# Optimization experiments

Hardware: AMD Instinct MI355X
Metric: run time of the kernel (lower is better)

The kernel has to match this reference:

```python
import jax, jax.numpy as jnp
import numpy as np

B, S, DM, H = 2, 2048, 1024, 16
D = DM // H
SCALE = D ** -0.5


def setup_inputs() -> dict:
    key = jax.random.key(0)
    k1, k2, k3 = jax.random.split(key, 3)
    x = jax.random.normal(k1, (B, S, DM), dtype=jnp.float32)
    w_qkv = jax.random.normal(k2, (DM, 3 * DM), dtype=jnp.float32) * (DM ** -0.5)
    b_qkv = jnp.zeros((3 * DM,), dtype=jnp.float32)
    w_out = jax.random.normal(k3, (DM, DM), dtype=jnp.float32) * (DM ** -0.5)
    b_out = jnp.zeros((DM,), dtype=jnp.float32)
    return {"x": x, "w_qkv": w_qkv, "b_qkv": b_qkv, "w_out": w_out, "b_out": b_out}


def reference(x, w_qkv, b_qkv, w_out, b_out):
    b, n, _ = x.shape
    qkv = x @ w_qkv + b_qkv                          # [b, n, 3*dm]
    q, k, v = jnp.split(qkv, 3, axis=-1)
    # b n (h d) -> b h n d
    split = lambda t: t.reshape(b, n, H, D).transpose(0, 2, 1, 3)
    q, k, v = split(q), split(k), split(v)
    dots = jnp.einsum('bhid,bhjd->bhij', q, k) * SCALE
    # causal (fore) mask: -inf above the diagonal
    causal = jnp.tril(jnp.ones((n, n), dtype=bool))
    dots = jnp.where(causal, dots, -jnp.inf)
    attn = jax.nn.softmax(dots, axis=-1)
    out = jnp.einsum('bhij,bhjd->bhid', attn, v)     # [b, h, n, d]
    out = out.transpose(0, 2, 1, 3).reshape(b, n, H * D)
    return out @ w_out + b_out
```

## Files before the change

kernel.cpp:

```cpp
#include <hip/hip_runtime.h>
#include <hip/hip_bf16.h>

#define NB 2
#define NS 2048
#define NDM 1024
#define NH 16
#define ND 64
#define NM (NB * NS)
#define RS 3072
#define C1 0.1803368801111243f
#define THR_RAW 44.36141956f

typedef __attribute__((ext_vector_type(8))) short bf16x8;
typedef __attribute__((ext_vector_type(4))) float f32x4;

__device__ __forceinline__ unsigned short f2bf(float f) {
    unsigned int u = __float_as_uint(f);
    u += 0x7fffu + ((u >> 16) & 1u);
    return (unsigned short)(u >> 16);
}

__device__ __forceinline__ void gload16(const unsigned short* g, unsigned short* l) {
    __builtin_amdgcn_global_load_lds(
        (const __attribute__((address_space(1))) void*)g,
        (__attribute__((address_space(3))) void*)l, 16, 0, 0);
}

__global__ __launch_bounds__(256)
void convert_bf16(const float* __restrict__ in, unsigned short* __restrict__ out, int n8) {
    int i = blockIdx.x * 256 + threadIdx.x;
    const int stride = gridDim.x * 256;
    for (; i < n8; i += stride) {
        const float4 a = ((const float4*)in)[i * 2];
        const float4 b = ((const float4*)in)[i * 2 + 1];
        bf16x8 v;
        v[0] = (short)f2bf(a.x); v[1] = (short)f2bf(a.y);
        v[2] = (short)f2bf(a.z); v[3] = (short)f2bf(a.w);
        v[4] = (short)f2bf(b.x); v[5] = (short)f2bf(b.y);
        v[6] = (short)f2bf(b.z); v[7] = (short)f2bf(b.w);
        *(bf16x8*)(out + (size_t)i * 8) = v;
    }
}

__global__ __launch_bounds__(256)
void transpose_bf16(const float* __restrict__ W, unsigned short* __restrict__ WT,
                    int K, int N) {
    __shared__ float Ts[64][65];
    const int n0 = blockIdx.x * 64, k0 = blockIdx.y * 64;
    const int t = threadIdx.x;
    {
        const int c4 = (t & 15) * 4;
        #pragma unroll
        for (int p = 0; p < 4; p++) {
            const int r = (t >> 4) + p * 16;
            const float4 v = *(const float4*)(W + (size_t)(k0 + r) * N + n0 + c4);
            Ts[r][c4] = v.x; Ts[r][c4 + 1] = v.y; Ts[r][c4 + 2] = v.z; Ts[r][c4 + 3] = v.w;
        }
    }
    __syncthreads();
    {
        const int cc8 = (t & 7) * 8;
        #pragma unroll
        for (int p = 0; p < 2; p++) {
            const int rr = (t >> 3) + p * 32;
            bf16x8 v;
            #pragma unroll
            for (int j = 0; j < 8; j++) v[j] = (short)f2bf(Ts[cc8 + j][rr]);
            *(bf16x8*)(WT + (size_t)(n0 + rr) * K + k0 + cc8) = v;
        }
    }
}

__global__ __launch_bounds__(256)
void vtrans(const unsigned short* __restrict__ qkvb, unsigned short* __restrict__ vT) {
    __shared__ unsigned short Ts[64][65];
    const int st = blockIdx.x, bh = blockIdx.y;
    const int h = bh & (NH - 1), b = bh >> 4;
    const int t = threadIdx.x;
    {
        const int c8 = (t & 7) * 8;
        #pragma unroll
        for (int p = 0; p < 2; p++) {
            const int r = (t >> 3) + p * 32;
            const unsigned short* src =
                qkvb + (size_t)(b * NS + st * 64 + r) * RS + 2 * NDM + h * ND + c8;
            const bf16x8 v = *(const bf16x8*)src;
            #pragma unroll
            for (int j = 0; j < 8; j++) Ts[r][c8 + j] = (unsigned short)v[j];
        }
    }
    __syncthreads();
    {
        #pragma unroll
        for (int i = 0; i < 2; i++) {
            const int u = t + i * 256;
            const int d = u >> 3, cg = (u & 7) * 8;
            bf16x8 v;
            #pragma unroll
            for (int j = 0; j < 8; j++) v[j] = (short)Ts[cg + j][d];
            *(bf16x8*)(vT + ((size_t)bh * ND + d) * NS + st * 64 + cg) = v;
        }
    }
}

template<int MODE>
__global__ __launch_bounds__(256)
void gemm128(const unsigned short* __restrict__ A, const unsigned short* __restrict__ BT,
             const float* __restrict__ bias, void* __restrict__ Cv,
             int M, int N, int K) {
    __shared__ unsigned short As[2][128 * 32];
    __shared__ unsigned short Bs[2][128 * 32];

    const int t = threadIdx.x, lane = t & 63, wv = t >> 6;
    const int wm = wv >> 1, wn = wv & 1;
    const int m0 = blockIdx.y * 128, n0 = blockIdx.x * 128;
    const int fr = lane & 15, fg = lane >> 4;

    f32x4 acc[4][4];
    #pragma unroll
    for (int m = 0; m < 4; m++)
        #pragma unroll
        for (int n = 0; n < 4; n++)
            #pragma unroll
            for (int r = 0; r < 4; r++) acc[m][n][r] = 0.f;

#define GSTAGE(buf, kk)                                                               \
    {                                                                                 \
        _Pragma("unroll")                                                             \
        for (int i = 0; i < 2; i++) {                                                 \
            const int u = t + i * 256;                                                \
            const int row = u >> 2;                                                   \
            const int grp = (u & 3) ^ ((row ^ (row >> 2)) & 3);                       \
            gload16(A  + (size_t)(m0 + row) * K + (kk) + grp * 8,                     \
                    &As[buf][(i * 256 + wv * 64) * 8]);                               \
            gload16(BT + (size_t)(n0 + row) * K + (kk) + grp * 8,                     \
                    &Bs[buf][(i * 256 + wv * 64) * 8]);                               \
        }                                                                             \
    }

#define GCOMPUTE(buf)                                                                 \
    {                                                                                 \
        bf16x8 af[4], bfv[4];                                                         \
        _Pragma("unroll")                                                             \
        for (int m = 0; m < 4; m++) {                                                 \
            const int row = wm * 64 + m * 16 + fr;                                    \
            af[m] = *(const bf16x8*)&As[buf][row * 32 +                               \
                        ((fg ^ ((row ^ (row >> 2)) & 3)) << 3)];                      \
        }                                                                             \
        _Pragma("unroll")                                                             \
        for (int n = 0; n < 4; n++) {                                                 \
            const int row = wn * 64 + n * 16 + fr;                                    \
            bfv[n] = *(const bf16x8*)&Bs[buf][row * 32 +                              \
                        ((fg ^ ((row ^ (row >> 2)) & 3)) << 3)];                      \
        }                                                                             \
        __builtin_amdgcn_s_setprio(1);                                                \
        _Pragma("unroll")                                                             \
        for (int m = 0; m < 4; m++)                                                   \
            _Pragma("unroll")                                                         \
            for (int n = 0; n < 4; n++)                                               \
                acc[m][n] = __builtin_amdgcn_mfma_f32_16x16x32_bf16(                  \
                    af[m], bfv[n], acc[m][n], 0, 0, 0);                               \
        __builtin_amdgcn_s_setprio(0);                                                \
    }

    GSTAGE(0, 0);
    for (int k0 = 0; k0 < K; k0 += 64) {
        __syncthreads();
        GSTAGE(1, k0 + 32);
        GCOMPUTE(0);
        __syncthreads();
        if (k0 + 64 < K) GSTAGE(0, k0 + 64);
        GCOMPUTE(1);
    }
#undef GSTAGE
#undef GCOMPUTE

    #pragma unroll
    for (int m = 0; m < 4; m++)
        #pragma unroll
        for (int n = 0; n < 4; n++) {
            const int col = n0 + wn * 64 + n * 16 + fr;
            const float bb = bias[col];
            #pragma unroll
            for (int rg = 0; rg < 4; rg++) {
                const int row = m0 + wm * 64 + m * 16 + fg * 4 + rg;
                const float v = acc[m][n][rg] + bb;
                if (MODE == 0) ((float*)Cv)[(size_t)row * N + col] = v;
                else ((unsigned short*)Cv)[(size_t)row * N + col] = f2bf(v);
            }
        }
}

__global__ __launch_bounds__(256)
void attn_mfma(const unsigned short* __restrict__ qkvb, const unsigned short* __restrict__ vT,
               unsigned short* __restrict__ atto) {
    const int bx = blockIdx.x;
    const int qt = (NS / 64 - 1) - (bx >> 5);
    const int bh = bx & 31;
    const int h = bh & (NH - 1), b = bh >> 4;
    const int q0 = qt * 64;
    const int t = threadIdx.x, lane = t & 63, wv = t >> 6;
    const int fr = lane & 15, fg = lane >> 4;

    __shared__ unsigned short Kt[2][128 * 64];
    __shared__ unsigned short Vt[2][64 * 128];
    __shared__ unsigned short Ps[4][16 * 128];

    const unsigned short* kb = qkvb + (size_t)b * NS * RS + NDM + h * ND;
    const unsigned short* vb = vT + (size_t)bh * ND * NS;

    bf16x8 qf[2];
    {
        const unsigned short* qrow =
            qkvb + (size_t)(b * NS + q0 + wv * 16 + fr) * RS + h * ND;
        qf[0] = *(const bf16x8*)(qrow + fg * 8);
        qf[1] = *(const bf16x8*)(qrow + 32 + fg * 8);
    }

    f32x4 oacc[4];
    #pragma unroll
    for (int d = 0; d < 4; d++)
        #pragma unroll
        for (int r = 0; r < 4; r++) oacc[d][r] = 0.f;
    float mrow[4] = {-INFINITY, -INFINITY, -INFINITY, -INFINITY};
    float nmC[4]  = {INFINITY, INFINITY, INFINITY, INFINITY};
    float lrow[4] = {0.f, 0.f, 0.f, 0.f};

    const int ntiles = (qt >> 1) + 1;

#define STAGE_KV(cbuf, jtile)                                                        \
    {                                                                                \
        _Pragma("unroll")                                                            \
        for (int i = 0; i < 4; i++) {                                                \
            const int u = t + i * 256;                                               \
            const int row = u >> 3;                                                  \
            const int grp = (u & 7) ^ (row & 7);                                     \
            gload16(kb + (size_t)((jtile) * 128 + row) * RS + grp * 8,               \
                    &Kt[cbuf][(i * 256 + wv * 64) * 8]);                             \
        }                                                                            \
        _Pragma("unroll")                                                            \
        for (int i = 0; i < 4; i++) {                                                \
            const int u = t + i * 256;                                               \
            const int row = u >> 4;                                                  \
            const int grp = (u & 15) ^ (row & 7);                                    \
            gload16(vb + (size_t)row * NS + (jtile) * 128 + grp * 8,                 \
                    &Vt[cbuf][(i * 256 + wv * 64) * 8]);                             \
        }                                                                            \
    }

    STAGE_KV(0, 0);

    for (int jt = 0; jt < ntiles; jt++) {
        const int cur = jt & 1;
        __syncthreads();
        if (jt + 1 < ntiles) STAGE_KV(cur ^ 1, jt + 1);
        const unsigned short* Ktc = Kt[cur];
        const unsigned short* Vtc = Vt[cur];

        f32x4 sacc[8];
        __builtin_amdgcn_s_setprio(1);
        #pragma unroll
        for (int kbi = 0; kbi < 8; kbi++) {
            #pragma unroll
            for (int r = 0; r < 4; r++) sacc[kbi][r] = 0.f;
            const int row = kbi * 16 + fr;
            const bf16x8 kf0 = *(const bf16x8*)&Ktc[row * 64 + (((fg) ^ (row & 7)) << 3)];
            const bf16x8 kf1 = *(const bf16x8*)&Ktc[row * 64 + (((4 + fg) ^ (row & 7)) << 3)];
            sacc[kbi] = __builtin_amdgcn_mfma_f32_16x16x32_bf16(qf[0], kf0, sacc[kbi], 0, 0, 0);
            sacc[kbi] = __builtin_amdgcn_mfma_f32_16x16x32_bf16(qf[1], kf1, sacc[kbi], 0, 0, 0);
        }
        __builtin_amdgcn_s_setprio(0);

        if (jt == ntiles - 1) {
            #pragma unroll
            for (int kbi = 0; kbi < 8; kbi++) {
                const int keyg = jt * 128 + kbi * 16 + fr;
                #pragma unroll
                for (int reg = 0; reg < 4; reg++) {
                    const int qg = q0 + wv * 16 + fg * 4 + reg;
                    if (keyg > qg) sacc[kbi][reg] = -INFINITY;
                }
            }
        }

        float pmax[4];
        #pragma unroll
        for (int reg = 0; reg < 4; reg++) {
            float pm = fmaxf(fmaxf(fmaxf(sacc[0][reg], sacc[1][reg]),
                                   fmaxf(sacc[2][reg], sacc[3][reg])),
                             fmaxf(fmaxf(sacc[4][reg], sacc[5][reg]),
                                   fmaxf(sacc[6][reg], sacc[7][reg])));
            pm = fmaxf(pm, __shfl_xor(pm, 1));
            pm = fmaxf(pm, __shfl_xor(pm, 2));
            pm = fmaxf(pm, __shfl_xor(pm, 4));
            pm = fmaxf(pm, __shfl_xor(pm, 8));
            pmax[reg] = pm;
        }
        bool need = false;
        #pragma unroll
        for (int reg = 0; reg < 4; reg++) need |= (pmax[reg] > mrow[reg] + THR_RAW);
        if (__any(need)) {
            #pragma unroll
            for (int reg = 0; reg < 4; reg++) {
                const float mn = fmaxf(mrow[reg], pmax[reg]);
                const float alpha = __builtin_amdgcn_exp2f((mrow[reg] - mn) * C1);
                mrow[reg] = mn;
                nmC[reg] = -mn * C1;
                lrow[reg] *= alpha;
                #pragma unroll
                for (int dblk = 0; dblk < 4; dblk++) oacc[dblk][reg] *= alpha;
            }
        }
        #pragma unroll
        for (int reg = 0; reg < 4; reg++) {
            float ps = 0.f;
            #pragma unroll
            for (int kbi = 0; kbi < 8; kbi++) {
                const float p = __builtin_amdgcn_exp2f(fmaf(sacc[kbi][reg], C1, nmC[reg]));
                sacc[kbi][reg] = p;
                ps += p;
            }
            ps += __shfl_xor(ps, 1);
            ps += __shfl_xor(ps, 2);
            ps += __shfl_xor(ps, 4);
            ps += __shfl_xor(ps, 8);
            lrow[reg] += ps;
        }

        #pragma unroll
        for (int kbi = 0; kbi < 8; kbi++) {
            const int colk = kbi * 16 + fr;
            #pragma unroll
            for (int reg = 0; reg < 4; reg++) {
                const int prow = fg * 4 + reg;
                Ps[wv][prow * 128 + (((colk >> 3) ^ (prow & 7)) << 3) + (colk & 7)] =
                    f2bf(sacc[kbi][reg]);
            }
        }

        bf16x8 pf[4];
        #pragma unroll
        for (int ks = 0; ks < 4; ks++)
            pf[ks] = *(const bf16x8*)&Ps[wv][fr * 128 + (((ks * 4 + fg) ^ (fr & 7)) << 3)];
        __builtin_amdgcn_s_setprio(1);
        #pragma unroll
        for (int dblk = 0; dblk < 4; dblk++) {
            const int vrow = dblk * 16 + fr;
            #pragma unroll
            for (int ks = 0; ks < 4; ks++) {
                const bf16x8 vf =
                    *(const bf16x8*)&Vtc[vrow * 128 + (((ks * 4 + fg) ^ (vrow & 7)) << 3)];
                oacc[dblk] = __builtin_amdgcn_mfma_f32_16x16x32_bf16(
                    pf[ks], vf, oacc[dblk], 0, 0, 0);
            }
        }
        __builtin_amdgcn_s_setprio(0);
    }
#undef STAGE_KV

    #pragma unroll
    for (int reg = 0; reg < 4; reg++) {
        const float inv = 1.f / lrow[reg];
        const int row = q0 + wv * 16 + fg * 4 + reg;
        unsigned short* dst = atto + ((size_t)b * NS + row) * NDM + h * ND;
        #pragma unroll
        for (int dblk = 0; dblk < 4; dblk++)
            dst[dblk * 16 + fr] = f2bf(oacc[dblk][reg] * inv);
    }
}

extern "C" void kernel_launch(void* const* d_in, const int* in_sizes, int n_in,
                              void* d_out, int out_size, void* d_ws, size_t ws_size,
                              hipStream_t stream) {
    const float* x     = (const float*)d_in[0];
    const float* w_qkv = (const float*)d_in[1];
    const float* b_qkv = (const float*)d_in[2];
    const float* w_out = (const float*)d_in[3];
    const float* b_out = (const float*)d_in[4];
    float* out = (float*)d_out;

    unsigned short* xb   = (unsigned short*)d_ws;
    unsigned short* wqT  = xb   + (size_t)NM * NDM;
    unsigned short* woT  = wqT  + (size_t)3 * NDM * NDM;
    unsigned short* qkvb = woT  + (size_t)NDM * NDM;
    unsigned short* vT   = qkvb + (size_t)NM * 3 * NDM;
    unsigned short* atto = xb;

    convert_bf16<<<2048, 256, 0, stream>>>(x, xb, NM * NDM / 8);
    transpose_bf16<<<dim3(3 * NDM / 64, NDM / 64), 256, 0, stream>>>(w_qkv, wqT, NDM, 3 * NDM);
    transpose_bf16<<<dim3(NDM / 64, NDM / 64), 256, 0, stream>>>(w_out, woT, NDM, NDM);

    gemm128<1><<<dim3(3 * NDM / 128, NM / 128), 256, 0, stream>>>(
        xb, wqT, b_qkv, qkvb, NM, 3 * NDM, NDM);

    vtrans<<<dim3(NS / 64, NB * NH), 256, 0, stream>>>(qkvb, vT);

    attn_mfma<<<dim3((NS / 64) * NB * NH), 256, 0, stream>>>(qkvb, vT, atto);

    gemm128<0><<<dim3(NDM / 128, NM / 128), 256, 0, stream>>>(
        atto, woT, b_out, out, NM, NDM, NDM);
}
```

Before: 205.9 us.

## Transpose QK^T MFMA so each lane owns one query row; narrow output GEMM tile

The QK^T MFMA operands are swapped so each lane's accumulator holds keys for a single query row. Row max and sum then need only two cross-lane shuffles instead of four per register, and the per-row softmax state collapses to scalars. The bf16 packing of P now uses v_cvt_pk_bf16_f32 with 32-bit LDS stores. The output projection switches to a new 128x64-tile GEMM, doubling its block count to improve CU occupancy on a grid that was small, at the cost of less operand reuse per block.

```diff
diff --git a/kernel.cpp b/kernel.cpp
--- a/kernel.cpp
+++ b/kernel.cpp
@@ -192,6 +192,95 @@
 }
 
 __global__ __launch_bounds__(256)
+void gemm128x64(const unsigned short* __restrict__ A, const unsigned short* __restrict__ BT,
+                const float* __restrict__ bias, float* __restrict__ C,
+                int M, int N, int K) {
+    __shared__ unsigned short As[2][128 * 32];
+    __shared__ unsigned short Bs[2][64 * 32];
+
+    const int t = threadIdx.x, lane = t & 63, wv = t >> 6;
+    const int wm = wv >> 1, wn = wv & 1;
+    const int m0 = blockIdx.y * 128, n0 = blockIdx.x * 64;
+    const int fr = lane & 15, fg = lane >> 4;
+
+    f32x4 acc[4][2];
+    #pragma unroll
+    for (int m = 0; m < 4; m++)
+        #pragma unroll
+        for (int n = 0; n < 2; n++)
+            #pragma unroll
+            for (int r = 0; r < 4; r++) acc[m][n][r] = 0.f;
+
+#define G2STAGE(buf, kk)                                                              \
+    {                                                                                 \
+        _Pragma("unroll")                                                             \
+        for (int i = 0; i < 2; i++) {                                                 \
+            const int u = t + i * 256;                                                \
+            const int row = u >> 2;                                                   \
+            const int grp = (u & 3) ^ ((row ^ (row >> 2)) & 3);                       \
+            gload16(A + (size_t)(m0 + row) * K + (kk) + grp * 8,                      \
+                    &As[buf][(i * 256 + wv * 64) * 8]);                               \
+        }                                                                             \
+        {                                                                             \
+            const int row = t >> 2;                                                   \
+            const int grp = (t & 3) ^ ((row ^ (row >> 2)) & 3);                       \
+            gload16(BT + (size_t)(n0 + row) * K + (kk) + grp * 8,                     \
+                    &Bs[buf][(wv * 64) * 8]);                                         \
+        }                                                                             \
+    }
+
+#define G2COMPUTE(buf)                                                                \
+    {                                                                                 \
+        bf16x8 af[4], bfv[2];                                                         \
+        _Pragma("unroll")                                                             \
+        for (int m = 0; m < 4; m++) {                                                 \
+            const int row = wm * 64 + m * 16 + fr;                                    \
+            af[m] = *(const bf16x8*)&As[buf][row * 32 +                               \
+                        ((fg ^ ((row ^ (row >> 2)) & 3)) << 3)];                      \
+        }                                                                             \
+        _Pragma("unroll")                                                             \
+        for (int n = 0; n < 2; n++) {                                                 \
+            const int row = wn * 32 + n * 16 + fr;                                    \
+            bfv[n] = *(const bf16x8*)&Bs[buf][row * 32 +                              \
+                        ((fg ^ ((row ^ (row >> 2)) & 3)) << 3)];                      \
+        }                                                                             \
+        __builtin_amdgcn_s_setprio(1);                                                \
+        _Pragma("unroll")                                                             \
+        for (int m = 0; m < 4; m++)                                                   \
+            _Pragma("unroll")                                                         \
+            for (int n = 0; n < 2; n++)                                               \
+                acc[m][n] = __builtin_amdgcn_mfma_f32_16x16x32_bf16(                  \
+                    af[m], bfv[n], acc[m][n], 0, 0, 0);                               \
+        __builtin_amdgcn_s_setprio(0);                                                \
+    }
+
+    G2STAGE(0, 0);
+    for (int k0 = 0; k0 < K; k0 += 64) {
+        __syncthreads();
+        G2STAGE(1, k0 + 32);
+        G2COMPUTE(0);
+        __syncthreads();
+        if (k0 + 64 < K) G2STAGE(0, k0 + 64);
+        G2COMPUTE(1);
+    }
+#undef G2STAGE
+#undef G2COMPUTE
+
+    #pragma unroll
+    for (int m = 0; m < 4; m++)
+        #pragma unroll
+        for (int n = 0; n < 2; n++) {
+            const int col = n0 + wn * 32 + n * 16 + fr;
+            const float bb = bias[col];
+            #pragma unroll
+            for (int rg = 0; rg < 4; rg++) {
+                const int row = m0 + wm * 64 + m * 16 + fg * 4 + rg;
+                C[(size_t)row * N + col] = acc[m][n][rg] + bb;
+            }
+        }
+}
+
+__global__ __launch_bounds__(256)
 void attn_mfma(const unsigned short* __restrict__ qkvb, const unsigned short* __restrict__ vT,
                unsigned short* __restrict__ atto) {
     const int bx = blockIdx.x;
@@ -222,9 +311,9 @@
     for (int d = 0; d < 4; d++)
         #pragma unroll
         for (int r = 0; r < 4; r++) oacc[d][r] = 0.f;
-    float mrow[4] = {-INFINITY, -INFINITY, -INFINITY, -INFINITY};
-    float nmC[4]  = {INFINITY, INFINITY, INFINITY, INFINITY};
-    float lrow[4] = {0.f, 0.f, 0.f, 0.f};
+    float mrow = -INFINITY;
+    float nmC  = INFINITY;
+    float lrow = 0.f;
 
     const int ntiles = (qt >> 1) + 1;
 
@@ -266,76 +355,72 @@
             const int row = kbi * 16 + fr;
             const bf16x8 kf0 = *(const bf16x8*)&Ktc[row * 64 + (((fg) ^ (row & 7)) << 3)];
             const bf16x8 kf1 = *(const bf16x8*)&Ktc[row * 64 + (((4 + fg) ^ (row & 7)) << 3)];
-            sacc[kbi] = __builtin_amdgcn_mfma_f32_16x16x32_bf16(qf[0], kf0, sacc[kbi], 0, 0, 0);
-            sacc[kbi] = __builtin_amdgcn_mfma_f32_16x16x32_bf16(qf[1], kf1, sacc[kbi], 0, 0, 0);
+            sacc[kbi] = __builtin_amdgcn_mfma_f32_16x16x32_bf16(kf0, qf[0], sacc[kbi], 0, 0, 0);
+            sacc[kbi] = __builtin_amdgcn_mfma_f32_16x16x32_bf16(kf1, qf[1], sacc[kbi], 0, 0, 0);
         }
         __builtin_amdgcn_s_setprio(0);
 
         if (jt == ntiles - 1) {
+            const int qg = q0 + wv * 16 + fr;
             #pragma unroll
             for (int kbi = 0; kbi < 8; kbi++) {
-                const int keyg = jt * 128 + kbi * 16 + fr;
                 #pragma unroll
                 for (int reg = 0; reg < 4; reg++) {
-                    const int qg = q0 + wv * 16 + fg * 4 + reg;
+                    const int keyg = jt * 128 + kbi * 16 + fg * 4 + reg;
                     if (keyg > qg) sacc[kbi][reg] = -INFINITY;
                 }
             }
         }
 
-        float pmax[4];
-        #pragma unroll
-        for (int reg = 0; reg < 4; reg++) {
-            float pm = fmaxf(fmaxf(fmaxf(sacc[0][reg], sacc[1][reg]),
-                                   fmaxf(sacc[2][reg], sacc[3][reg])),
-                             fmaxf(fmaxf(sacc[4][reg], sacc[5][reg]),
-                                   fmaxf(sacc[6][reg], sacc[7][reg])));
-            pm = fmaxf(pm, __shfl_xor(pm, 1));
-            pm = fmaxf(pm, __shfl_xor(pm, 2));
-            pm = fmaxf(pm, __shfl_xor(pm, 4));
-            pm = fmaxf(pm, __shfl_xor(pm, 8));
-            pmax[reg] = pm;
-        }
-        bool need = false;
-        #pragma unroll
-        for (int reg = 0; reg < 4; reg++) need |= (pmax[reg] > mrow[reg] + THR_RAW);
-        if (__any(need)) {
+        float mk[8];
+        #pragma unroll
+        for (int kbi = 0; kbi < 8; kbi++)
+            mk[kbi] = fmaxf(fmaxf(sacc[kbi][0], sacc[kbi][1]),
+                            fmaxf(sacc[kbi][2], sacc[kbi][3]));
+        float pm = fmaxf(fmaxf(fmaxf(mk[0], mk[1]), fmaxf(mk[2], mk[3])),
+                         fmaxf(fmaxf(mk[4], mk[5]), fmaxf(mk[6], mk[7])));
+        pm = fmaxf(pm, __shfl_xor(pm, 16));
+        pm = fmaxf(pm, __shfl_xor(pm, 32));
+
+        if (__any(pm > mrow + THR_RAW)) {
+            const float mn = fmaxf(mrow, pm);
+            const float alpha = __builtin_amdgcn_exp2f((mrow - mn) * C1);
+            mrow = mn;
+            nmC = -mn * C1;
+            lrow *= alpha;
             #pragma unroll
             for (int reg = 0; reg < 4; reg++) {
-                const float mn = fmaxf(mrow[reg], pmax[reg]);
-                const float alpha = __builtin_amdgcn_exp2f((mrow[reg] - mn) * C1);
-                mrow[reg] = mn;
-                nmC[reg] = -mn * C1;
-                lrow[reg] *= alpha;
+                const float aq = __shfl(alpha, fg * 4 + reg);
                 #pragma unroll
-                for (int dblk = 0; dblk < 4; dblk++) oacc[dblk][reg] *= alpha;
-            }
-        }
-        #pragma unroll
-        for (int reg = 0; reg < 4; reg++) {
-            float ps = 0.f;
-            #pragma unroll
-            for (int kbi = 0; kbi < 8; kbi++) {
-                const float p = __builtin_amdgcn_exp2f(fmaf(sacc[kbi][reg], C1, nmC[reg]));
+                for (int dblk = 0; dblk < 4; dblk++) oacc[dblk][reg] *= aq;
+            }
+        }
+
+        float psum = 0.f;
+        #pragma unroll
+        for (int kbi = 0; kbi < 8; kbi++) {
+            #pragma unroll
+            for (int reg = 0; reg < 4; reg++) {
+                const float p = __builtin_amdgcn_exp2f(fmaf(sacc[kbi][reg], C1, nmC));
                 sacc[kbi][reg] = p;
-                ps += p;
-            }
-            ps += __shfl_xor(ps, 1);
-            ps += __shfl_xor(ps, 2);
-            ps += __shfl_xor(ps, 4);
-            ps += __shfl_xor(ps, 8);
-            lrow[reg] += ps;
-        }
+                psum += p;
+            }
+        }
+        psum += __shfl_xor(psum, 16);
+        psum += __shfl_xor(psum, 32);
+        lrow += psum;
 
         #pragma unroll
         for (int kbi = 0; kbi < 8; kbi++) {
-            const int colk = kbi * 16 + fr;
-            #pragma unroll
-            for (int reg = 0; reg < 4; reg++) {
-                const int prow = fg * 4 + reg;
-                Ps[wv][prow * 128 + (((colk >> 3) ^ (prow & 7)) << 3) + (colk & 7)] =
-                    f2bf(sacc[kbi][reg]);
-            }
+            unsigned int w0, w1;
+            asm("v_cvt_pk_bf16_f32 %0, %1, %2"
+                : "=v"(w0) : "v"(sacc[kbi][0]), "v"(sacc[kbi][1]));
+            asm("v_cvt_pk_bf16_f32 %0, %1, %2"
+                : "=v"(w1) : "v"(sacc[kbi][2]), "v"(sacc[kbi][3]));
+            const int grp = (kbi * 2 + (fg >> 1)) ^ (fr & 7);
+            const int base = fr * 128 + grp * 8 + (fg & 1) * 4;
+            *(unsigned int*)&Ps[wv][base]     = w0;
+            *(unsigned int*)&Ps[wv][base + 2] = w1;
         }
 
         bf16x8 pf[4];
@@ -358,9 +443,10 @@
     }
 #undef STAGE_KV
 
+    const float rl = 1.f / lrow;
     #pragma unroll
     for (int reg = 0; reg < 4; reg++) {
-        const float inv = 1.f / lrow[reg];
+        const float inv = __shfl(rl, fg * 4 + reg);
         const int row = q0 + wv * 16 + fg * 4 + reg;
         unsigned short* dst = atto + ((size_t)b * NS + row) * NDM + h * ND;
         #pragma unroll
@@ -397,6 +483,6 @@
 
     attn_mfma<<<dim3((NS / 64) * NB * NH), 256, 0, stream>>>(qkvb, vT, atto);
 
-    gemm128<0><<<dim3(NDM / 128, NM / 128), 256, 0, stream>>>(
+    gemm128x64<<<dim3(NDM / 64, NM / 128), 256, 0, stream>>>(
         atto, woT, b_out, out, NM, NDM, NDM);
 }
```

Result: faster. 185.2 us (-10.0%).
